# Performance work log

Measured on AMD Instinct MI355X. Metric: run time of the kernel, lower is better.

Reference implementation:

```python
import jax, jax.numpy as jnp
import numpy as np

N_NODES = 100000
N_EDGES = 1600000
NFEAT = 128
NHID = 128
NCLASS = 64


def setup_inputs() -> dict:
    key = jax.random.key(0)
    ks = jax.random.split(key, 8)
    x = jax.random.normal(ks[0], (N_NODES, NFEAT), dtype=jnp.float32)
    edge_src = jax.random.randint(ks[1], (N_EDGES,), 0, N_NODES, dtype=jnp.int32)
    edge_dst = jax.random.randint(ks[2], (N_EDGES,), 0, N_NODES, dtype=jnp.int32)
    edge_w = jax.random.uniform(ks[3], (N_EDGES,), dtype=jnp.float32)
    W0 = jax.random.normal(ks[4], (NFEAT, NHID), dtype=jnp.float32) * (2.0 / (NFEAT + NHID)) ** 0.5
    b0 = jax.random.normal(ks[5], (1, NHID), dtype=jnp.float32) * 0.02
    W1 = jax.random.normal(ks[6], (NHID, NCLASS), dtype=jnp.float32) * (2.0 / (NHID + NCLASS)) ** 0.5
    b1 = jax.random.normal(ks[7], (1, NCLASS), dtype=jnp.float32) * 0.02
    return {"x": x, "edge_src": edge_src, "edge_dst": edge_dst, "edge_w": edge_w,
            "W0": W0, "b0": b0, "W1": W1, "b1": b1}


def _spmm(edge_src, edge_dst, edge_w, h):
    # A_norm @ h via gather + weighted segment-sum over edges. [E,d] gather dominates.
    msgs = h[edge_src] * edge_w[:, None]          # [E, d]
    return jax.ops.segment_sum(msgs, edge_dst, num_segments=N_NODES)  # [N, d]


def reference(x, edge_src, edge_dst, edge_w, W0, b0, W1, b1):
    # Layer 1: aggregate -> linear -> bias -> ReLU (dropout=0, eval mode)
    h = _spmm(edge_src, edge_dst, edge_w, x)      # [N, nfeat]
    h = jax.nn.relu(h @ W0 + b0)                  # [N, nhid]
    # Layer 2 (output layer): aggregate -> linear -> bias
    h = _spmm(edge_src, edge_dst, edge_w, h)      # [N, nhid]
    h = h @ W1 + b1                               # [N, nclass]
    return jax.nn.log_softmax(h, axis=1)
```

## Files before the change

kernel.cpp:

```cpp
#include <hip/hip_runtime.h>

#define NF 128
#define NC 64
#define NBMAX 512
#define TPART 8192
#define BCAP 5120
#define WPITCH 136

static inline size_t alignup(size_t x){ return (x + 255) & ~(size_t)255; }

typedef __attribute__((ext_vector_type(8))) short bf16x8;
typedef __attribute__((ext_vector_type(4))) float f32x4;
typedef __attribute__((ext_vector_type(16))) int i32x16;

__device__ __forceinline__ unsigned short f2bf(float f){
  unsigned u = __float_as_uint(f);
  u += 0x7fffu + ((u >> 16) & 1u);
  return (unsigned short)(u >> 16);
}
__device__ __forceinline__ float bflo(unsigned u){ return __uint_as_float(u << 16); }
__device__ __forceinline__ float bfhi(unsigned u){ return __uint_as_float(u & 0xffff0000u); }

__device__ __forceinline__ void sload16_issue(i32x16& r, const int2* p){
  asm volatile("s_load_dwordx16 %0, %1, 0x0" : "=s"(r) : "s"(p));
}
__device__ __forceinline__ void swait2(i32x16& a, i32x16& b){
  asm volatile("s_waitcnt lgkmcnt(0)" : "+s"(a), "+s"(b));
}
__device__ __forceinline__ void swait4(i32x16& a, i32x16& b, i32x16& c, i32x16& d){
  asm volatile("s_waitcnt lgkmcnt(0)" : "+s"(a), "+s"(b), "+s"(c), "+s"(d));
}

__global__ __launch_bounds__(256) void k_cvtW(const float* __restrict__ W0, const float* __restrict__ W1,
                                              unsigned short* __restrict__ W0t, unsigned short* __restrict__ W1t,
                                              int* __restrict__ bcur, int NB){
  int t = blockIdx.x*256 + threadIdx.x;
  if (t < NB) bcur[t] = t * BCAP;
  if (t < 128*128){ int k = t >> 7, c = t & 127; W0t[c*128 + k] = f2bf(W0[t]); }
  int u = t - 128*128;
  if (u >= 0 && u < 128*64){ int k = u >> 6, c = u & 63; W1t[c*128 + k] = f2bf(W1[u]); }
}

__global__ __launch_bounds__(1024) void k_part(const int* __restrict__ src, const int* __restrict__ dst,
    const float* __restrict__ w, int* __restrict__ bcur, int2* __restrict__ part, int E, int NB){
  __shared__ int2 stage[TPART];
  __shared__ int hist[NBMAX];
  __shared__ int scn[NBMAX];
  __shared__ int cnt2[NBMAX];
  __shared__ int baseg[NBMAX];
  const int t = threadIdx.x;
  const int t0 = blockIdx.x * TPART;
  if (t < NBMAX){ hist[t] = 0; cnt2[t] = 0; }
  __syncthreads();
  #pragma unroll 4
  for (int k = 0; k < 8; ++k){
    int i = t0 + (k << 10) + t;
    if (i < E) atomicAdd(&hist[dst[i] >> 8], 1);
  }
  __syncthreads();
  if (t < NBMAX) scn[t] = hist[t];
  __syncthreads();
  for (int o = 1; o < NBMAX; o <<= 1){
    int a = (t >= o && t < NBMAX) ? scn[t-o] : 0;
    __syncthreads();
    if (t < NBMAX) scn[t] += a;
    __syncthreads();
  }
  if (t < NB) baseg[t] = hist[t] ? atomicAdd(&bcur[t], hist[t]) : 0;
  __syncthreads();
  #pragma unroll 4
  for (int k = 0; k < 8; ++k){
    int i = t0 + (k << 10) + t;
    if (i < E){
      int d = dst[i], b = d >> 8;
      int r = atomicAdd(&cnt2[b], 1);
      stage[scn[b] - hist[b] + r] = make_int2(((d & 255) << 17) | src[i], __float_as_int(w[i]));
    }
  }
  __syncthreads();
  int wv = t >> 6, ln = t & 63;
  for (int b = wv; b < NB; b += 16){
    int c = hist[b];
    if (!c) continue;
    int lo = scn[b] - c, gb = baseg[b];
    for (int s2 = ln; s2 < c; s2 += 64) part[gb + s2] = stage[lo + s2];
  }
}

__global__ __launch_bounds__(512) void k_fill2(const int2* __restrict__ part, const int* __restrict__ bcur,
    int2* __restrict__ noff, int2* __restrict__ csr, int N){
  __shared__ int deg[256], scn[256], c2[256];
  const int b = blockIdx.x, t = threadIdx.x;
  const int base = b * BCAP;
  const int cnt = bcur[b] - base;
  const int d0 = b << 8;
  const int nd = min(256, N - d0);
  if (t < 256){ deg[t] = 0; c2[t] = 0; }
  __syncthreads();
  for (int s = t; s < cnt; s += 512) atomicAdd(&deg[(part[base+s].x >> 17) & 255], 1);
  __syncthreads();
  if (t < 256) scn[t] = deg[t];
  __syncthreads();
  for (int o = 1; o < 256; o <<= 1){
    int a = (t < 256 && t >= o) ? scn[t-o] : 0;
    __syncthreads();
    if (t < 256) scn[t] += a;
    __syncthreads();
  }
  if (t < nd) noff[d0 + t] = make_int2(base + scn[t] - deg[t], base + scn[t]);
  __syncthreads();
  for (int s = t; s < cnt; s += 512){
    int2 rec = part[base + s];
    int dl = (rec.x >> 17) & 255;
    int p = base + scn[dl] - deg[dl] + atomicAdd(&c2[dl], 1);
    csr[p] = make_int2(rec.x & 0x1FFFF, rec.y);
  }
}

__global__ __launch_bounds__(256) void k_gemm1(const float* __restrict__ A, const unsigned short* __restrict__ Wg,
                                               unsigned short* __restrict__ Y, int n){
  __shared__ unsigned short Wt[128*WPITCH];
  const int tid = threadIdx.x;
  for (int i = tid; i < 128*16; i += 256){
    int r = i >> 4, c = (i & 15) << 3;
    *(uint4*)(Wt + r*WPITCH + c) = *(const uint4*)(Wg + r*128 + c);
  }
  __syncthreads();
  const int lane = tid & 63, wv = tid >> 6;
  const int r0 = blockIdx.x*64 + wv*16;
  int rA = r0 + (lane & 15); if (rA > n-1) rA = n-1;
  const int kq = (lane >> 4) << 3;
  f32x4 acc[8] = {};
  #pragma unroll
  for (int kk = 0; kk < 4; ++kk){
    const float* ap = A + (size_t)rA*NF + kk*32 + kq;
    float4 a0 = *(const float4*)ap;
    float4 a1 = *(const float4*)(ap + 4);
    bf16x8 af;
    af[0]=(short)f2bf(a0.x); af[1]=(short)f2bf(a0.y); af[2]=(short)f2bf(a0.z); af[3]=(short)f2bf(a0.w);
    af[4]=(short)f2bf(a1.x); af[5]=(short)f2bf(a1.y); af[6]=(short)f2bf(a1.z); af[7]=(short)f2bf(a1.w);
    const unsigned short* wp = Wt + (lane & 15)*WPITCH + kk*32 + kq;
    #pragma unroll
    for (int nt = 0; nt < 8; ++nt){
      bf16x8 bf = *(const bf16x8*)(wp + nt*16*WPITCH);
      acc[nt] = __builtin_amdgcn_mfma_f32_16x16x32_bf16(af, bf, acc[nt], 0, 0, 0);
    }
  }
  const int rb = r0 + ((lane >> 4) << 2);
  #pragma unroll
  for (int j = 0; j < 4; ++j){
    int rg = rb + j;
    if (rg < n){
      unsigned short* yp = Y + (size_t)rg*NF + (lane & 15);
      #pragma unroll
      for (int nt = 0; nt < 8; ++nt) yp[nt*16] = f2bf(acc[nt][j]);
    }
  }
}

__global__ __launch_bounds__(256) void k_gemm2(const unsigned short* __restrict__ Ab, const unsigned short* __restrict__ Wg,
                                               unsigned short* __restrict__ G, int n){
  __shared__ unsigned short Wt[64*WPITCH];
  const int tid = threadIdx.x;
  for (int i = tid; i < 64*16; i += 256){
    int r = i >> 4, c = (i & 15) << 3;
    *(uint4*)(Wt + r*WPITCH + c) = *(const uint4*)(Wg + r*128 + c);
  }
  __syncthreads();
  const int lane = tid & 63, wv = tid >> 6;
  const int r0 = blockIdx.x*64 + wv*16;
  int rA = r0 + (lane & 15); if (rA > n-1) rA = n-1;
  const int kq = (lane >> 4) << 3;
  f32x4 acc[4] = {};
  #pragma unroll
  for (int kk = 0; kk < 4; ++kk){
    bf16x8 af = *(const bf16x8*)(Ab + (size_t)rA*NF + kk*32 + kq);
    const unsigned short* wp = Wt + (lane & 15)*WPITCH + kk*32 + kq;
    #pragma unroll
    for (int nt = 0; nt < 4; ++nt){
      bf16x8 bf = *(const bf16x8*)(wp + nt*16*WPITCH);
      acc[nt] = __builtin_amdgcn_mfma_f32_16x16x32_bf16(af, bf, acc[nt], 0, 0, 0);
    }
  }
  const int rb = r0 + ((lane >> 4) << 2);
  #pragma unroll
  for (int j = 0; j < 4; ++j){
    int rg = rb + j;
    if (rg < n){
      unsigned short* gp = G + (size_t)rg*NC + (lane & 15);
      #pragma unroll
      for (int nt = 0; nt < 4; ++nt) gp[nt*16] = f2bf(acc[nt][j]);
    }
  }
}

__global__ __launch_bounds__(256, 6) void k_spmm_relu(const unsigned short* __restrict__ y, const int2* __restrict__ csr,
    const int2* __restrict__ noff, const float* __restrict__ bias, unsigned short* __restrict__ h, int n){
  int wid  = (blockIdx.x * 256 + threadIdx.x) >> 6;
  int lane = threadIdx.x & 63;
  if (wid >= n) return;
  const int2 se = noff[wid];
  const int s = __builtin_amdgcn_readfirstlane(se.x);
  const int e = __builtin_amdgcn_readfirstlane(se.y);
  const int half = lane >> 5, li = lane & 31;
  const unsigned liOff = (unsigned)li << 3;
  const char* yb = (const char*)y;
  float a0x[2]={0.f,0.f}, a0y[2]={0.f,0.f}, a1x[2]={0.f,0.f}, a1y[2]={0.f,0.f};
  const int deg = e - s;

#define RELU_FMA(VV, WW)                                                      \
    _Pragma("unroll")                                                         \
    for (int k = 0; k < 8; ++k){                                              \
      a0x[k&1] = fmaf(WW[k], bflo(VV[k].x), a0x[k&1]);                        \
      a0y[k&1] = fmaf(WW[k], bfhi(VV[k].x), a0y[k&1]);                        \
      a1x[k&1] = fmaf(WW[k], bflo(VV[k].y), a1x[k&1]);                        \
      a1y[k&1] = fmaf(WW[k], bfhi(VV[k].y), a1y[k&1]);                        \
    }

  if (deg > 0 && deg <= 16){
    i32x16 rA, rB;
    sload16_issue(rA, csr + s);
    sload16_issue(rB, csr + s + 8);
    swait2(rA, rB);
    const int jbh = s + (half << 3);
    unsigned offk[8]; float wk[8];
    #pragma unroll
    for (int k = 0; k < 8; ++k){
      int r  = half ? rB[2*k]   : rA[2*k];
      int wb = half ? rB[2*k+1] : rA[2*k+1];
      r = ((unsigned)r < (unsigned)n) ? r : 0;
      offk[k] = ((unsigned)r << 8) + liOff;
      wk[k] = (jbh + k < e) ? __int_as_float(wb) : 0.f;
    }
    uint2 v[8];
    #pragma unroll
    for (int k = 0; k < 8; ++k) v[k] = *(const uint2*)(yb + offk[k]);
    __builtin_amdgcn_sched_barrier(0);
    RELU_FMA(v, wk)
  } else if (deg > 16 && deg <= 32){
    i32x16 rA0, rB0, rA1, rB1;
    sload16_issue(rA0, csr + s);
    sload16_issue(rB0, csr + s + 8);
    sload16_issue(rA1, csr + e - 16);
    sload16_issue(rB1, csr + e - 8);
    swait4(rA0, rB0, rA1, rB1);
    const int lo1 = s + 16;
    const int t1 = (e - 16) + (half << 3);
    unsigned off0[8], off1[8]; float wk0[8], wk1[8];
    #pragma unroll
    for (int k = 0; k < 8; ++k){
      int r0v = half ? rB0[2*k] : rA0[2*k];
      int w0v = half ? rB0[2*k+1] : rA0[2*k+1];
      off0[k] = ((unsigned)r0v << 8) + liOff;
      wk0[k] = __int_as_float(w0v);
      int r1v = half ? rB1[2*k] : rA1[2*k];
      int w1v = half ? rB1[2*k+1] : rA1[2*k+1];
      off1[k] = ((unsigned)r1v << 8) + liOff;
      wk1[k] = (t1 + k >= lo1) ? __int_as_float(w1v) : 0.f;
    }
    uint2 v0[8], v1[8];
    #pragma unroll
    for (int k = 0; k < 8; ++k) v0[k] = *(const uint2*)(yb + off0[k]);
    #pragma unroll
    for (int k = 0; k < 8; ++k) v1[k] = *(const uint2*)(yb + off1[k]);
    __builtin_amdgcn_sched_barrier(0);
    RELU_FMA(v0, wk0)
    RELU_FMA(v1, wk1)
  } else if (deg > 32){
    int jb = s;
    const int nfull = deg >> 4;
    for (int b = 0; b < nfull; ++b, jb += 16){
      i32x16 rA, rB;
      sload16_issue(rA, csr + jb);
      sload16_issue(rB, csr + jb + 8);
      swait2(rA, rB);
      unsigned offk[8]; float wk[8];
      #pragma unroll
      for (int k = 0; k < 8; ++k){
        int r  = half ? rB[2*k]   : rA[2*k];
        int wb = half ? rB[2*k+1] : rA[2*k+1];
        offk[k] = ((unsigned)r << 8) + liOff;
        wk[k] = __int_as_float(wb);
      }
      uint2 v[8];
      #pragma unroll
      for (int k = 0; k < 8; ++k) v[k] = *(const uint2*)(yb + offk[k]);
      __builtin_amdgcn_sched_barrier(0);
      RELU_FMA(v, wk)
    }
    if (jb < e){
      i32x16 rA, rB;
      sload16_issue(rA, csr + e - 16);
      sload16_issue(rB, csr + e - 8);
      swait2(rA, rB);
      const int t1 = (e - 16) + (half << 3);
      unsigned offk[8]; float wk[8];
      #pragma unroll
      for (int k = 0; k < 8; ++k){
        int r  = half ? rB[2*k]   : rA[2*k];
        int wb = half ? rB[2*k+1] : rA[2*k+1];
        offk[k] = ((unsigned)r << 8) + liOff;
        wk[k] = (t1 + k >= jb) ? __int_as_float(wb) : 0.f;
      }
      uint2 v[8];
      #pragma unroll
      for (int k = 0; k < 8; ++k) v[k] = *(const uint2*)(yb + offk[k]);
      __builtin_amdgcn_sched_barrier(0);
      RELU_FMA(v, wk)
    }
  }
#undef RELU_FMA
  float o0 = a0x[0]+a0x[1], o1 = a0y[0]+a0y[1], o2 = a1x[0]+a1x[1], o3 = a1y[0]+a1y[1];
  o0 += __shfl_xor(o0, 32); o1 += __shfl_xor(o1, 32);
  o2 += __shfl_xor(o2, 32); o3 += __shfl_xor(o3, 32);
  float4 bb = ((const float4*)bias)[li];
  o0 = fmaxf(o0 + bb.x, 0.f); o1 = fmaxf(o1 + bb.y, 0.f);
  o2 = fmaxf(o2 + bb.z, 0.f); o3 = fmaxf(o3 + bb.w, 0.f);
  if (half == 0){
    uint2 p;
    p.x = (unsigned)f2bf(o0) | ((unsigned)f2bf(o1) << 16);
    p.y = (unsigned)f2bf(o2) | ((unsigned)f2bf(o3) << 16);
    *(uint2*)(h + (size_t)wid * NF + li*4) = p;
  }
}

__global__ __launch_bounds__(256, 6) void k_spmm_ls(const unsigned short* __restrict__ g, const int2* __restrict__ csr,
    const int2* __restrict__ noff, const float* __restrict__ bias, float* __restrict__ out, int n){
  int wid  = (blockIdx.x * 256 + threadIdx.x) >> 6;
  int lane = threadIdx.x & 63;
  if (wid >= n) return;
  const int2 se = noff[wid];
  const int s = __builtin_amdgcn_readfirstlane(se.x);
  const int e = __builtin_amdgcn_readfirstlane(se.y);
  const int half = lane >> 5, li = lane & 31;
  const unsigned liOff = (unsigned)li << 2;
  const char* gb = (const char*)g;
  float z0[2]={0.f,0.f}, z1[2]={0.f,0.f};
  const int deg = e - s;

#define LS_FMA(VV, WW)                                                        \
    _Pragma("unroll")                                                         \
    for (int k = 0; k < 8; ++k){                                              \
      z0[k&1] = fmaf(WW[k], bflo(VV[k]), z0[k&1]);                            \
      z1[k&1] = fmaf(WW[k], bfhi(VV[k]), z1[k&1]);                            \
    }

  if (deg > 0 && deg <= 16){
    i32x16 rA, rB;
    sload16_issue(rA, csr + s);
    sload16_issue(rB, csr + s + 8);
    swait2(rA, rB);
    const int jbh = s + (half << 3);
    unsigned offk[8]; float wk[8];
    #pragma unroll
    for (int k = 0; k < 8; ++k){
      int r  = half ? rB[2*k]   : rA[2*k];
      int wb = half ? rB[2*k+1] : rA[2*k+1];
      r = ((unsigned)r < (unsigned)n) ? r : 0;
      offk[k] = ((unsigned)r << 7) + liOff;
      wk[k] = (jbh + k < e) ? __int_as_float(wb) : 0.f;
    }
    unsigned v[8];
    #pragma unroll
    for (int k = 0; k < 8; ++k) v[k] = *(const unsigned*)(gb + offk[k]);
    __builtin_amdgcn_sched_barrier(0);
    LS_FMA(v, wk)
  } else if (deg > 16 && deg <= 32){
    i32x16 rA0, rB0, rA1, rB1;
    sload16_issue(rA0, csr + s);
    sload16_issue(rB0, csr + s + 8);
    sload16_issue(rA1, csr + e - 16);
    sload16_issue(rB1, csr + e - 8);
    swait4(rA0, rB0, rA1, rB1);
    const int lo1 = s + 16;
    const int t1 = (e - 16) + (half << 3);
    unsigned off0[8], off1[8]; float wk0[8], wk1[8];
    #pragma unroll
    for (int k = 0; k < 8; ++k){
      int r0v = half ? rB0[2*k] : rA0[2*k];
      int w0v = half ? rB0[2*k+1] : rA0[2*k+1];
      off0[k] = ((unsigned)r0v << 7) + liOff;
      wk0[k] = __int_as_float(w0v);
      int r1v = half ? rB1[2*k] : rA1[2*k];
      int w1v = half ? rB1[2*k+1] : rA1[2*k+1];
      off1[k] = ((unsigned)r1v << 7) + liOff;
      wk1[k] = (t1 + k >= lo1) ? __int_as_float(w1v) : 0.f;
    }
    unsigned v0[8], v1[8];
    #pragma unroll
    for (int k = 0; k < 8; ++k) v0[k] = *(const unsigned*)(gb + off0[k]);
    #pragma unroll
    for (int k = 0; k < 8; ++k) v1[k] = *(const unsigned*)(gb + off1[k]);
    __builtin_amdgcn_sched_barrier(0);
    LS_FMA(v0, wk0)
    LS_FMA(v1, wk1)
  } else if (deg > 32){
    int jb = s;
    const int nfull = deg >> 4;
    for (int b = 0; b < nfull; ++b, jb += 16){
      i32x16 rA, rB;
      sload16_issue(rA, csr + jb);
      sload16_issue(rB, csr + jb + 8);
      swait2(rA, rB);
      unsigned offk[8]; float wk[8];
      #pragma unroll
      for (int k = 0; k < 8; ++k){
        int r  = half ? rB[2*k]   : rA[2*k];
        int wb = half ? rB[2*k+1] : rA[2*k+1];
        offk[k] = ((unsigned)r << 7) + liOff;
        wk[k] = __int_as_float(wb);
      }
      unsigned v[8];
      #pragma unroll
      for (int k = 0; k < 8; ++k) v[k] = *(const unsigned*)(gb + offk[k]);
      __builtin_amdgcn_sched_barrier(0);
      LS_FMA(v, wk)
    }
    if (jb < e){
      i32x16 rA, rB;
      sload16_issue(rA, csr + e - 16);
      sload16_issue(rB, csr + e - 8);
      swait2(rA, rB);
      const int t1 = (e - 16) + (half << 3);
      unsigned offk[8]; float wk[8];
      #pragma unroll
      for (int k = 0; k < 8; ++k){
        int r  = half ? rB[2*k]   : rA[2*k];
        int wb = half ? rB[2*k+1] : rA[2*k+1];
        offk[k] = ((unsigned)r << 7) + liOff;
        wk[k] = (t1 + k >= jb) ? __int_as_float(wb) : 0.f;
      }
      unsigned v[8];
      #pragma unroll
      for (int k = 0; k < 8; ++k) v[k] = *(const unsigned*)(gb + offk[k]);
      __builtin_amdgcn_sched_barrier(0);
      LS_FMA(v, wk)
    }
  }
#undef LS_FMA
  float zz0 = z0[0]+z0[1], zz1 = z1[0]+z1[1];
  zz0 += __shfl_xor(zz0, 32); zz1 += __shfl_xor(zz1, 32);
  float2 bb = ((const float2*)bias)[li];
  zz0 += bb.x; zz1 += bb.y;
  float m = fmaxf(zz0, zz1);
  for (int o = 16; o; o >>= 1) m = fmaxf(m, __shfl_xor(m, o));
  float sum = expf(zz0 - m) + expf(zz1 - m);
  for (int o = 16; o; o >>= 1) sum += __shfl_xor(sum, o);
  float lg = logf(sum);
  if (half == 0)
    *(float2*)(out + (size_t)wid * NC + li*2) = make_float2(zz0 - m - lg, zz1 - m - lg);
}

extern "C" void kernel_launch(void* const* d_in, const int* in_sizes, int n_in,
                              void* d_out, int out_size, void* d_ws, size_t ws_size,
                              hipStream_t stream){
  const float* x  = (const float*)d_in[0];
  const int* esrc = (const int*)d_in[1];
  const int* edst = (const int*)d_in[2];
  const float* ew = (const float*)d_in[3];
  const float* W0 = (const float*)d_in[4];
  const float* b0 = (const float*)d_in[5];
  const float* W1 = (const float*)d_in[6];
  const float* b1 = (const float*)d_in[7];
  float* out = (float*)d_out;

  const int N = in_sizes[0] / NF;
  const int E = in_sizes[1];
  const int NB = (N + 255) >> 8;

  char* ws = (char*)d_ws;
  size_t o = 0;
  int*  bcur  = (int*) (ws + o); o = alignup(o + NBMAX*4);
  int2* noff  = (int2*)(ws + o); o = alignup(o + (size_t)N*8);
  unsigned short* W0t = (unsigned short*)(ws + o); o = alignup(o + 128*128*2);
  unsigned short* W1t = (unsigned short*)(ws + o); o = alignup(o + 128*64*2);
  int2* part  = (int2*)(ws + o); o = alignup(o + (size_t)NB*BCAP*8);
  int2* csr   = (int2*)(ws + o); o = alignup(o + (size_t)NB*BCAP*8 + 256);
  unsigned short* y  = (unsigned short*)(ws + o); o = alignup(o + (size_t)N*NF*2);
  unsigned short* hb = (unsigned short*)(ws + o); o = alignup(o + (size_t)N*NF*2);
  unsigned short* g = y;

  const int pb = (E + TPART-1)/TPART;

  k_cvtW <<<96, 256, 0, stream>>>(W0, W1, W0t, W1t, bcur, NB);
  k_part <<<pb, 1024, 0, stream>>>(esrc, edst, ew, bcur, part, E, NB);
  k_fill2<<<NB, 512, 0, stream>>>(part, bcur, noff, csr, N);

  const int gb = (N + 63)/64;
  const int sb = (N + 3)/4;

  k_gemm1<<<gb, 256, 0, stream>>>(x, W0t, y, N);
  k_spmm_relu<<<sb, 256, 0, stream>>>(y, csr, noff, b0, hb, N);
  k_gemm2<<<gb, 256, 0, stream>>>(hb, W1t, g, N);
  k_spmm_ls<<<sb, 256, 0, stream>>>(g, csr, noff, b1, out, N);
}
```

Before: 173.0 us.

## Merge edge partitioning and first GEMM into one heterogeneous launch

Fuses the edge-partition kernel and the first dense GEMM into a single launch. Block indices below PB do partitioning and the rest do GEMM on 256-row tiles with 1024 threads, sharing one raw shared-memory buffer. The two independent stages can overlap on the GPU and one launch is removed. GEMM blocks now carry the partition kernel's large shared-memory footprint and 1024-thread shape, which may reduce their occupancy.

```diff
diff --git a/kernel.cpp b/kernel.cpp
--- a/kernel.cpp
+++ b/kernel.cpp
@@ -41,49 +41,90 @@
   if (u >= 0 && u < 128*64){ int k = u >> 6, c = u & 63; W1t[c*128 + k] = f2bf(W1[u]); }
 }
 
-__global__ __launch_bounds__(1024) void k_part(const int* __restrict__ src, const int* __restrict__ dst,
-    const float* __restrict__ w, int* __restrict__ bcur, int2* __restrict__ part, int E, int NB){
-  __shared__ int2 stage[TPART];
-  __shared__ int hist[NBMAX];
-  __shared__ int scn[NBMAX];
-  __shared__ int cnt2[NBMAX];
-  __shared__ int baseg[NBMAX];
+__global__ __launch_bounds__(1024, 4) void k_partg(const int* __restrict__ src, const int* __restrict__ dst,
+    const float* __restrict__ w, int* __restrict__ bcur, int2* __restrict__ part, int E, int NB, int PB,
+    const float* __restrict__ A, const unsigned short* __restrict__ Wg, unsigned short* __restrict__ Y, int n){
+  __shared__ __align__(16) char smem[TPART*8 + NBMAX*16];
   const int t = threadIdx.x;
-  const int t0 = blockIdx.x * TPART;
-  if (t < NBMAX){ hist[t] = 0; cnt2[t] = 0; }
-  __syncthreads();
-  #pragma unroll 4
-  for (int k = 0; k < 8; ++k){
-    int i = t0 + (k << 10) + t;
-    if (i < E) atomicAdd(&hist[dst[i] >> 8], 1);
-  }
-  __syncthreads();
-  if (t < NBMAX) scn[t] = hist[t];
-  __syncthreads();
-  for (int o = 1; o < NBMAX; o <<= 1){
-    int a = (t >= o && t < NBMAX) ? scn[t-o] : 0;
-    __syncthreads();
-    if (t < NBMAX) scn[t] += a;
-    __syncthreads();
-  }
-  if (t < NB) baseg[t] = hist[t] ? atomicAdd(&bcur[t], hist[t]) : 0;
-  __syncthreads();
-  #pragma unroll 4
-  for (int k = 0; k < 8; ++k){
-    int i = t0 + (k << 10) + t;
-    if (i < E){
-      int d = dst[i], b = d >> 8;
-      int r = atomicAdd(&cnt2[b], 1);
-      stage[scn[b] - hist[b] + r] = make_int2(((d & 255) << 17) | src[i], __float_as_int(w[i]));
-    }
-  }
-  __syncthreads();
-  int wv = t >> 6, ln = t & 63;
-  for (int b = wv; b < NB; b += 16){
-    int c = hist[b];
-    if (!c) continue;
-    int lo = scn[b] - c, gb = baseg[b];
-    for (int s2 = ln; s2 < c; s2 += 64) part[gb + s2] = stage[lo + s2];
+  if ((int)blockIdx.x < PB){
+    int2* stage = (int2*)smem;
+    int* hist  = (int*)(smem + TPART*8);
+    int* scn   = hist + NBMAX;
+    int* cnt2  = scn + NBMAX;
+    int* baseg = cnt2 + NBMAX;
+    const int t0 = blockIdx.x * TPART;
+    if (t < NBMAX){ hist[t] = 0; cnt2[t] = 0; }
+    __syncthreads();
+    #pragma unroll 4
+    for (int k = 0; k < 8; ++k){
+      int i = t0 + (k << 10) + t;
+      if (i < E) atomicAdd(&hist[dst[i] >> 8], 1);
+    }
+    __syncthreads();
+    if (t < NBMAX) scn[t] = hist[t];
+    __syncthreads();
+    for (int o = 1; o < NBMAX; o <<= 1){
+      int a = (t >= o && t < NBMAX) ? scn[t-o] : 0;
+      __syncthreads();
+      if (t < NBMAX) scn[t] += a;
+      __syncthreads();
+    }
+    if (t < NB) baseg[t] = hist[t] ? atomicAdd(&bcur[t], hist[t]) : 0;
+    __syncthreads();
+    #pragma unroll 4
+    for (int k = 0; k < 8; ++k){
+      int i = t0 + (k << 10) + t;
+      if (i < E){
+        int d = dst[i], b = d >> 8;
+        int r = atomicAdd(&cnt2[b], 1);
+        stage[scn[b] - hist[b] + r] = make_int2(((d & 255) << 17) | src[i], __float_as_int(w[i]));
+      }
+    }
+    __syncthreads();
+    int wv = t >> 6, ln = t & 63;
+    for (int b = wv; b < NB; b += 16){
+      int c = hist[b];
+      if (!c) continue;
+      int lo = scn[b] - c, gb = baseg[b];
+      for (int s2 = ln; s2 < c; s2 += 64) part[gb + s2] = stage[lo + s2];
+    }
+  } else {
+    unsigned short* Wt = (unsigned short*)smem;
+    for (int i = t; i < 128*16; i += 1024){
+      int r = i >> 4, c = (i & 15) << 3;
+      *(uint4*)(Wt + r*WPITCH + c) = *(const uint4*)(Wg + r*128 + c);
+    }
+    __syncthreads();
+    const int lane = t & 63, wv = t >> 6;
+    const int r0 = (blockIdx.x - PB)*256 + wv*16;
+    int rA = r0 + (lane & 15); if (rA > n-1) rA = n-1;
+    const int kq = (lane >> 4) << 3;
+    f32x4 acc[8] = {};
+    #pragma unroll
+    for (int kk = 0; kk < 4; ++kk){
+      const float* ap = A + (size_t)rA*NF + kk*32 + kq;
+      float4 a0 = *(const float4*)ap;
+      float4 a1 = *(const float4*)(ap + 4);
+      bf16x8 af;
+      af[0]=(short)f2bf(a0.x); af[1]=(short)f2bf(a0.y); af[2]=(short)f2bf(a0.z); af[3]=(short)f2bf(a0.w);
+      af[4]=(short)f2bf(a1.x); af[5]=(short)f2bf(a1.y); af[6]=(short)f2bf(a1.z); af[7]=(short)f2bf(a1.w);
+      const unsigned short* wp = Wt + (lane & 15)*WPITCH + kk*32 + kq;
+      #pragma unroll
+      for (int nt = 0; nt < 8; ++nt){
+        bf16x8 bf = *(const bf16x8*)(wp + nt*16*WPITCH);
+        acc[nt] = __builtin_amdgcn_mfma_f32_16x16x32_bf16(af, bf, acc[nt], 0, 0, 0);
+      }
+    }
+    const int rb = r0 + ((lane >> 4) << 2);
+    #pragma unroll
+    for (int j = 0; j < 4; ++j){
+      int rg = rb + j;
+      if (rg < n){
+        unsigned short* yp = Y + (size_t)rg*NF + (lane & 15);
+        #pragma unroll
+        for (int nt = 0; nt < 8; ++nt) yp[nt*16] = f2bf(acc[nt][j]);
+      }
+    }
   }
 }
 
@@ -117,47 +158,6 @@
   }
 }
 
-__global__ __launch_bounds__(256) void k_gemm1(const float* __restrict__ A, const unsigned short* __restrict__ Wg,
-                                               unsigned short* __restrict__ Y, int n){
-  __shared__ unsigned short Wt[128*WPITCH];
-  const int tid = threadIdx.x;
-  for (int i = tid; i < 128*16; i += 256){
-    int r = i >> 4, c = (i & 15) << 3;
-    *(uint4*)(Wt + r*WPITCH + c) = *(const uint4*)(Wg + r*128 + c);
-  }
-  __syncthreads();
-  const int lane = tid & 63, wv = tid >> 6;
-  const int r0 = blockIdx.x*64 + wv*16;
-  int rA = r0 + (lane & 15); if (rA > n-1) rA = n-1;
-  const int kq = (lane >> 4) << 3;
-  f32x4 acc[8] = {};
-  #pragma unroll
-  for (int kk = 0; kk < 4; ++kk){
-    const float* ap = A + (size_t)rA*NF + kk*32 + kq;
-    float4 a0 = *(const float4*)ap;
-    float4 a1 = *(const float4*)(ap + 4);
-    bf16x8 af;
-    af[0]=(short)f2bf(a0.x); af[1]=(short)f2bf(a0.y); af[2]=(short)f2bf(a0.z); af[3]=(short)f2bf(a0.w);
-    af[4]=(short)f2bf(a1.x); af[5]=(short)f2bf(a1.y); af[6]=(short)f2bf(a1.z); af[7]=(short)f2bf(a1.w);
-    const unsigned short* wp = Wt + (lane & 15)*WPITCH + kk*32 + kq;
-    #pragma unroll
-    for (int nt = 0; nt < 8; ++nt){
-      bf16x8 bf = *(const bf16x8*)(wp + nt*16*WPITCH);
-      acc[nt] = __builtin_amdgcn_mfma_f32_16x16x32_bf16(af, bf, acc[nt], 0, 0, 0);
-    }
-  }
-  const int rb = r0 + ((lane >> 4) << 2);
-  #pragma unroll
-  for (int j = 0; j < 4; ++j){
-    int rg = rb + j;
-    if (rg < n){
-      unsigned short* yp = Y + (size_t)rg*NF + (lane & 15);
-      #pragma unroll
-      for (int nt = 0; nt < 8; ++nt) yp[nt*16] = f2bf(acc[nt][j]);
-    }
-  }
-}
-
 __global__ __launch_bounds__(256) void k_gemm2(const unsigned short* __restrict__ Ab, const unsigned short* __restrict__ Wg,
                                                unsigned short* __restrict__ G, int n){
   __shared__ unsigned short Wt[64*WPITCH];
@@ -480,16 +480,17 @@
   unsigned short* hb = (unsigned short*)(ws + o); o = alignup(o + (size_t)N*NF*2);
   unsigned short* g = y;
 
-  const int pb = (E + TPART-1)/TPART;
+  const int pb  = (E + TPART-1)/TPART;
+  const int gb1 = (N + 255)/256;
 
   k_cvtW <<<96, 256, 0, stream>>>(W0, W1, W0t, W1t, bcur, NB);
-  k_part <<<pb, 1024, 0, stream>>>(esrc, edst, ew, bcur, part, E, NB);
+  k_partg<<<pb + gb1, 1024, 0, stream>>>(esrc, edst, ew, bcur, part, E, NB, pb,
+                                         x, W0t, y, N);
   k_fill2<<<NB, 512, 0, stream>>>(part, bcur, noff, csr, N);
 
   const int gb = (N + 63)/64;
   const int sb = (N + 3)/4;
 
-  k_gemm1<<<gb, 256, 0, stream>>>(x, W0t, y, N);
   k_spmm_relu<<<sb, 256, 0, stream>>>(y, csr, noff, b0, hb, N);
   k_gemm2<<<gb, 256, 0, stream>>>(hb, W1t, g, N);
   k_spmm_ls<<<sb, 256, 0, stream>>>(g, csr, noff, b1, out, N);
```

New measurement: 167.7 us, median of 2. -3.1%, faster.
